# Performance work log

Hardware: AMD Instinct MI355X
Metric: run time of the kernel (lower is better)

## Reference

```python
import jax, jax.numpy as jnp
import numpy as np


def setup_inputs() -> dict:
    key = jax.random.key(0)
    k1, k2 = jax.random.split(key)
    queries = jax.random.normal(k1, (16, 1024, 256), dtype=jnp.float32)
    embedding = jax.random.normal(k2, (8192, 256), dtype=jnp.float32) * 0.02
    return {"queries": queries, "embedding": embedding}


def reference(queries, embedding):
    commitment_weight = 0.25
    # squared L2 distances: ||q||^2 + ||e||^2 - 2 q.e  -> [b, k, n]
    q_sq = jnp.sum(queries * queries, axis=-1, keepdims=True)          # [b,k,1]
    e_sq = jnp.sum(embedding * embedding, axis=-1)[None, None, :]      # [1,1,n]
    distances = q_sq + e_sq - 2.0 * jnp.einsum('bkc,nc->bkn', queries, embedding)
    code_indices = jnp.argmin(distances, axis=-1)                      # [b,k] int
    quantized = embedding[code_indices]                                # [b,k,c]
    commit_loss = jnp.mean((jax.lax.stop_gradient(queries) - quantized) ** 2)
    codebook_loss = jnp.mean((queries - jax.lax.stop_gradient(quantized)) ** 2)
    vq_loss = codebook_loss + commitment_weight * commit_loss
    # straight-through estimator
    quantized_st = queries + jax.lax.stop_gradient(quantized - queries)
    return (code_indices, quantized_st, vq_loss)
```

## Files before the change

### kernel.cpp

```cpp
#include <hip/hip_runtime.h>
#include <float.h>

typedef _Float16 half8 __attribute__((ext_vector_type(8)));
typedef _Float16 half4v __attribute__((ext_vector_type(4)));
typedef float f32x4 __attribute__((ext_vector_type(4)));

#define M_TOTAL 16384
#define N_CODES 8192
#define KDIM    256
#define BM 128
#define BN 256
#define BK 32
#define NK (KDIM / BK)
#define NB (N_CODES / BN)
#define TS 32
#define MARGIN 3.6e-3f
#define SQ_SCALE 512.0f
#define SE_SCALE 2048.0f
#define INV_PROD 1.9073486328125e-06f
#define RB 1024
#define LR_BLOCKS 32

#define PREP_Q_BLOCKS (M_TOTAL / 4)
#define PREP_E_BLOCKS (N_CODES / 4)
#define TR_BLOCKS ((N_CODES / 64) * (KDIM / 64))

__device__ __forceinline__ void prep_body(const float* __restrict__ src,
                                          _Float16* __restrict__ dst,
                                          float* __restrict__ sq, float scale,
                                          int row0, int tid) {
    {
        const int r = row0 + (tid >> 6);
        const int e4 = tid & 63;
        const float4 v = *(const float4*)(src + (size_t)r * KDIM + e4 * 4);
        const half4v h = {(_Float16)(v.x * scale), (_Float16)(v.y * scale),
                          (_Float16)(v.z * scale), (_Float16)(v.w * scale)};
        ((half4v*)(dst + (size_t)r * KDIM))[e4] = h;
    }
    if (tid < 64) {
        const int grp = tid >> 4;
        const int sub = tid & 15;
        const int row = row0 + grp;
        const float* p = src + (size_t)row * KDIM + (sub >> 3) * 128 + (sub & 7);
        float r;
        {
            #pragma clang fp contract(off)
            float v = p[0];
            r = v * v;
            #pragma unroll
            for (int k = 1; k < 16; k++) { const float w = p[k * 8]; r = r + w * w; }
        }
        const float t1 = r  + __shfl_xor(r,  1, 64);
        const float t2 = t1 + __shfl_xor(t1, 2, 64);
        const float t3 = t2 + __shfl_xor(t2, 4, 64);
        const float t4 = t3 + __shfl_xor(t3, 8, 64);
        if (sub == 0) sq[row] = t4;
    }
}

__global__ void prep_fused_kernel(const float* __restrict__ Q, const float* __restrict__ E,
                                  _Float16* __restrict__ Qh, _Float16* __restrict__ Eh,
                                  float* __restrict__ qsq, float* __restrict__ esq,
                                  float* __restrict__ ET,
                                  int* __restrict__ fcount, float* __restrict__ loss_slot) {
    __shared__ float tile[64][65];
    const int tid = threadIdx.x;
    const int b = blockIdx.x;
    if (b == 0 && tid == 0) { *fcount = 0; *loss_slot = 0.f; }
    if (b < PREP_Q_BLOCKS) {
        prep_body(Q, Qh, qsq, SQ_SCALE, b * 4, tid);
        return;
    }
    if (b < PREP_Q_BLOCKS + PREP_E_BLOCKS) {
        prep_body(E, Eh, esq, SE_SCALE, (b - PREP_Q_BLOCKS) * 4, tid);
        return;
    }
    const int idx = b - PREP_Q_BLOCKS - PREP_E_BLOCKS;
    const int n0 = (idx & 127) * 64;
    const int k0 = (idx >> 7) * 64;
    const int r = tid >> 4;
    const int c4 = tid & 15;
    #pragma unroll
    for (int p = 0; p < 4; p++) {
        const int row = p * 16 + r;
        const float4 v = *(const float4*)(E + (size_t)(n0 + row) * KDIM + k0 + c4 * 4);
        tile[row][c4 * 4 + 0] = v.x;
        tile[row][c4 * 4 + 1] = v.y;
        tile[row][c4 * 4 + 2] = v.z;
        tile[row][c4 * 4 + 3] = v.w;
    }
    __syncthreads();
    #pragma unroll
    for (int p = 0; p < 4; p++) {
        const int d = p * 16 + r;
        float4 o;
        o.x = tile[c4 * 4 + 0][d];
        o.y = tile[c4 * 4 + 1][d];
        o.z = tile[c4 * 4 + 2][d];
        o.w = tile[c4 * 4 + 3][d];
        *(float4*)(ET + (size_t)(k0 + d) * N_CODES + n0 + c4 * 4) = o;
    }
}

union SMemU {
    struct { _Float16 q[3][BM * TS]; _Float16 e[3][BN * TS]; } t;
    struct { unsigned k1[BM][2]; unsigned k2[BM][2]; } red;
};

__device__ __forceinline__ void gl_lds16(const void* g, void* lds) {
    __builtin_amdgcn_global_load_lds(
        (const __attribute__((address_space(1))) unsigned*)g,
        (__attribute__((address_space(3))) unsigned*)lds, 16, 0, 0);
}

__global__ __launch_bounds__(256, 2)
void mfma_top2_kernel(const _Float16* __restrict__ Qh, const _Float16* __restrict__ Eh,
                      const float* __restrict__ esq,
                      unsigned* __restrict__ k1s, unsigned* __restrict__ k2s) {
    __shared__ SMemU sm;
    const int tid = threadIdx.x;
    const int m0 = blockIdx.x * BM;
    const int n0 = blockIdx.y * BN;
    const int w = tid >> 6, lane = tid & 63;
    const int wm = w >> 1, wn = w & 1;
    const int qd = lane >> 4, c = lane & 15;

    const int lrow = lane >> 2;
    const int gsw = (lane & 3) ^ ((lane >> 3) & 3);
    const _Float16* qsrc = Qh + (size_t)(m0 + w * 32 + lrow) * KDIM + gsw * 8;
    const _Float16* esrc = Eh + (size_t)(n0 + w * 64 + lrow) * KDIM + gsw * 8;

    f32x4 acc[4][8];
    const f32x4 zero = {0.f, 0.f, 0.f, 0.f};
    #pragma unroll
    for (int mt = 0; mt < 4; mt++)
        #pragma unroll
        for (int nt = 0; nt < 8; nt++) acc[mt][nt] = zero;

    #define STAGE(buf, kofs) do {                                                  \
        _Float16* qdst = sm.t.q[buf] + w * 1024;                                   \
        _Float16* edst = sm.t.e[buf] + w * 2048;                                   \
        gl_lds16(qsrc + (kofs),             qdst);                                 \
        gl_lds16(qsrc + 16 * KDIM + (kofs), qdst + 512);                           \
        gl_lds16(esrc + (kofs),             edst);                                 \
        gl_lds16(esrc + 16 * KDIM + (kofs), edst + 512);                           \
        gl_lds16(esrc + 32 * KDIM + (kofs), edst + 1024);                          \
        gl_lds16(esrc + 48 * KDIM + (kofs), edst + 1536);                          \
    } while (0)

    STAGE(0, 0);
    STAGE(1, BK);
    STAGE(2, 2 * BK);
    asm volatile("s_waitcnt vmcnt(12)" ::: "memory");
    __builtin_amdgcn_s_barrier();

    const int csw = (c >> 1) & 3;

    #pragma unroll
    for (int ki = 0; ki < NK; ki++) {
        const int buf = ki % 3;
        const _Float16* bq = sm.t.q[buf];
        const _Float16* be = sm.t.e[buf];
        half8 qa[4];
        #pragma unroll
        for (int mt = 0; mt < 4; mt++)
            qa[mt] = *(const half8*)(bq + (wm * 64 + mt * 16 + c) * TS + (qd ^ csw) * 8);
        __builtin_amdgcn_s_setprio(1);
        #pragma unroll
        for (int nt = 0; nt < 8; nt++) {
            const half8 eh = *(const half8*)(be + (wn * 128 + nt * 16 + c) * TS + (qd ^ csw) * 8);
            #pragma unroll
            for (int mt = 0; mt < 4; mt++)
                acc[mt][nt] = __builtin_amdgcn_mfma_f32_16x16x32_f16(qa[mt], eh, acc[mt][nt], 0, 0, 0);
        }
        __builtin_amdgcn_s_setprio(0);
        if (ki == NK - 1) break;
        if (ki <= NK - 3) { asm volatile("s_waitcnt vmcnt(6)" ::: "memory"); }
        else              { asm volatile("s_waitcnt vmcnt(0)" ::: "memory"); }
        __builtin_amdgcn_s_barrier();
        if (ki + 3 < NK) STAGE(buf, (ki + 3) * BK);
    }
    #undef STAGE

    float es8[8];
    #pragma unroll
    for (int nt = 0; nt < 8; nt++) es8[nt] = esq[n0 + wn * 128 + nt * 16 + c] + 8.0f;

    unsigned k1[16], k2[16];
    #pragma unroll
    for (int i = 0; i < 16; i++) { k1[i] = 0xFFFFFFFFu; k2[i] = 0xFFFFFFFFu; }

    #pragma unroll
    for (int mt = 0; mt < 4; mt++)
        #pragma unroll
        for (int nt = 0; nt < 8; nt++) {
            const unsigned nl = (unsigned)(wn * 128 + nt * 16 + c);
            #pragma unroll
            for (int r = 0; r < 4; r++) {
                const int i = mt * 4 + r;
                const float d = fmaf(acc[mt][nt][r], -INV_PROD, es8[nt]);
                const unsigned k = (__float_as_uint(d) & 0xFFFFFF00u) | nl;
                const unsigned t = min(k1[i], k);
                k2[i] = min(k2[i], max(k1[i], k));
                k1[i] = t;
            }
        }
    #pragma unroll
    for (int s = 1; s < 16; s <<= 1) {
        #pragma unroll
        for (int i = 0; i < 16; i++) {
            const unsigned ok1 = (unsigned)__shfl_xor((int)k1[i], s, 64);
            const unsigned ok2 = (unsigned)__shfl_xor((int)k2[i], s, 64);
            const unsigned t = min(k1[i], ok1);
            k2[i] = min(min(k2[i], ok2), max(k1[i], ok1));
            k1[i] = t;
        }
    }
    __syncthreads();
    if (c == 0) {
        #pragma unroll
        for (int mt = 0; mt < 4; mt++)
            #pragma unroll
            for (int r = 0; r < 4; r++) {
                const int ml = wm * 64 + mt * 16 + qd * 4 + r;
                sm.red.k1[ml][wn] = k1[mt * 4 + r];
                sm.red.k2[ml][wn] = k2[mt * 4 + r];
            }
    }
    __syncthreads();
    if (tid < BM) {
        const unsigned a1 = sm.red.k1[tid][0], b1 = sm.red.k1[tid][1];
        const unsigned a2 = sm.red.k2[tid][0], b2 = sm.red.k2[tid][1];
        const size_t o = (size_t)(m0 + tid) * NB + blockIdx.y;
        k1s[o] = min(a1, b1);
        k2s[o] = min(min(a2, b2), max(a1, b1));
    }
}

__global__ void finalize_kernel(const float* __restrict__ Q, const float* __restrict__ E,
                                const unsigned* __restrict__ k1s, const unsigned* __restrict__ k2s,
                                int* __restrict__ fcount, int* __restrict__ flist,
                                float* __restrict__ ws_loss, float* __restrict__ out) {
    const int q = blockIdx.x * 4 + (threadIdx.x >> 6);
    const int lane = threadIdx.x & 63;
    unsigned d1 = 0xFFFFFF00u;
    unsigned d2 = 0xFFFFFF00u;
    int gi = 0x7FFFFFFF;
    if (lane < NB) {
        const unsigned k1 = k1s[(size_t)q * NB + lane];
        const unsigned k2 = k2s[(size_t)q * NB + lane];
        d1 = k1 & 0xFFFFFF00u;
        gi = lane * BN + (int)(k1 & 255u);
        d2 = k2 & 0xFFFFFF00u;
    }
    #pragma unroll
    for (int s = 1; s < 64; s <<= 1) {
        const unsigned od1 = (unsigned)__shfl_xor((int)d1, s, 64);
        const int      ogi = __shfl_xor(gi, s, 64);
        const unsigned od2 = (unsigned)__shfl_xor((int)d2, s, 64);
        const unsigned nd2 = min(min(d2, od2), max(d1, od1));
        const bool take = (od1 < d1) || (od1 == d1 && ogi < gi);
        d1 = take ? od1 : d1;
        gi = take ? ogi : gi;
        d2 = nd2;
    }
    if ((__uint_as_float(d2) - __uint_as_float(d1)) < MARGIN) {
        if (lane == 0) flist[atomicAdd(fcount, 1)] = q;
        return;
    }

    if (lane == 0) out[q] = (float)gi;
    const float4 qv = *(const float4*)(Q + (size_t)q * KDIM + lane * 4);
    const float4 ev = *(const float4*)(E + (size_t)gi * KDIM + lane * 4);
    float4 st;
    {
        #pragma clang fp contract(off)
        st.x = qv.x + (ev.x - qv.x);
        st.y = qv.y + (ev.y - qv.y);
        st.z = qv.z + (ev.z - qv.z);
        st.w = qv.w + (ev.w - qv.w);
    }
    *(float4*)(out + M_TOTAL + (size_t)q * KDIM + lane * 4) = st;

    const float dx = qv.x - ev.x, dy = qv.y - ev.y, dz = qv.z - ev.z, dw = qv.w - ev.w;
    float s = dx * dx + dy * dy + dz * dz + dw * dw;
    #pragma unroll
    for (int off = 32; off > 0; off >>= 1) s += __shfl_down(s, off);
    if (lane == 0) ws_loss[q] = s;
}

__global__ __launch_bounds__(256, 4)
void refine_kernel(const float* __restrict__ Q, const float* __restrict__ E,
                   const float* __restrict__ ET,
                   const float* __restrict__ qsq, const float* __restrict__ esq,
                   const int* __restrict__ fcount, const int* __restrict__ flist,
                   const unsigned* __restrict__ k1s,
                   float* __restrict__ ws_loss, float* __restrict__ out) {
    const int cnt = *fcount;
    const int tid = threadIdx.x;
    const int w = tid >> 6, lane = tid & 63;
    __shared__ float qs[KDIM];
    __shared__ unsigned cmask_sh;
    __shared__ float redv[4];
    __shared__ int   redi[4];

    for (int fi = blockIdx.x; fi < cnt; fi += RB) {
        const int q = flist[fi];
        __syncthreads();
        qs[tid] = Q[(size_t)q * KDIM + tid];
        if (w == 0) {
            unsigned k1 = 0xFFFFFF00u;
            if (lane < NB) k1 = k1s[(size_t)q * NB + lane];
            unsigned m = k1;
            #pragma unroll
            for (int s = 1; s < 64; s <<= 1)
                m = min(m, (unsigned)__shfl_xor((int)m, s, 64));
            const float thr = __uint_as_float(m & 0xFFFFFF00u) + MARGIN;
            const bool cand = (lane < NB) &&
                              (__uint_as_float(k1 & 0xFFFFFF00u) < thr);
            const unsigned long long bal = __ballot(cand);
            if (lane == 0) cmask_sh = (unsigned)bal;
        }
        __syncthreads();
        unsigned cmask = cmask_sh;
        const float qsv = qsq[q];
        float bv = FLT_MAX;
        int   bi = 0x7fffffff;
        while (cmask) {
            const int cb = __builtin_ctz(cmask);
            cmask &= cmask - 1;
            const int n = cb * BN + tid;
            float a = 0.f;
            #pragma unroll 8
            for (int k = 0; k < KDIM; k++)
                a = fmaf(qs[k], ET[(size_t)k * N_CODES + n], a);
            float d;
            {
                #pragma clang fp contract(off)
                const float t1 = qsv + esq[n];
                d = t1 - 2.0f * a;
            }
            if (d < bv || (d == bv && n < bi)) { bv = d; bi = n; }
        }
        #pragma unroll
        for (int s = 1; s < 64; s <<= 1) {
            const float ov = __shfl_xor(bv, s, 64);
            const int   oi = __shfl_xor(bi, s, 64);
            if (ov < bv || (ov == bv && oi < bi)) { bv = ov; bi = oi; }
        }
        if (lane == 0) { redv[w] = bv; redi[w] = bi; }
        __syncthreads();
        float fv = redv[0]; int fidx = redi[0];
        #pragma unroll
        for (int u = 1; u < 4; u++) {
            if (redv[u] < fv || (redv[u] == fv && redi[u] < fidx)) {
                fv = redv[u]; fidx = redi[u];
            }
        }
        if (w == 0) {
            if (lane == 0) out[q] = (float)fidx;
            const float4 qv = *(const float4*)(Q + (size_t)q * KDIM + lane * 4);
            const float4 ev = *(const float4*)(E + (size_t)fidx * KDIM + lane * 4);
            float4 st;
            {
                #pragma clang fp contract(off)
                st.x = qv.x + (ev.x - qv.x);
                st.y = qv.y + (ev.y - qv.y);
                st.z = qv.z + (ev.z - qv.z);
                st.w = qv.w + (ev.w - qv.w);
            }
            *(float4*)(out + M_TOTAL + (size_t)q * KDIM + lane * 4) = st;
            const float dx = qv.x - ev.x, dy = qv.y - ev.y;
            const float dz = qv.z - ev.z, dw = qv.w - ev.w;
            float s = dx * dx + dy * dy + dz * dz + dw * dw;
            #pragma unroll
            for (int off = 32; off > 0; off >>= 1) s += __shfl_down(s, off);
            if (lane == 0) ws_loss[q] = s;
        }
    }
}

__global__ void loss_reduce_kernel(const float* __restrict__ ws_loss, float* __restrict__ out) {
    const int tid = threadIdx.x;
    float s = 0.f;
    for (int i = blockIdx.x * 256 + tid; i < M_TOTAL; i += LR_BLOCKS * 256)
        s += ws_loss[i];
    #pragma unroll
    for (int off = 32; off > 0; off >>= 1) s += __shfl_down(s, off);
    __shared__ float ws[4];
    if ((tid & 63) == 0) ws[tid >> 6] = s;
    __syncthreads();
    if (tid == 0) {
        const float tot = (ws[0] + ws[1]) + (ws[2] + ws[3]);
        atomicAdd(out + M_TOTAL + (size_t)M_TOTAL * KDIM,
                  tot * (1.25f / (float)((size_t)M_TOTAL * KDIM)));
    }
}

extern "C" void kernel_launch(void* const* d_in, const int* in_sizes, int n_in,
                              void* d_out, int out_size, void* d_ws, size_t ws_size,
                              hipStream_t stream) {
    const float* Q = (const float*)d_in[0];
    const float* E = (const float*)d_in[1];
    float* out = (float*)d_out;

    char* ws = (char*)d_ws;
    _Float16* Qh  = (_Float16*)(ws);
    _Float16* Eh  = (_Float16*)(ws + (size_t)8  * 1024 * 1024);
    float* qsq    = (float*)   (ws + (size_t)12 * 1024 * 1024);
    float* esq    = qsq + M_TOTAL;
    unsigned* k1s = (unsigned*)(ws + (size_t)13 * 1024 * 1024);
    unsigned* k2s = (unsigned*)(ws + (size_t)17 * 1024 * 1024);
    int*   fcount = (int*)     (ws + (size_t)25 * 1024 * 1024);
    int*   flist  = fcount + 64;
    float* ws_loss= (float*)   (ws + (size_t)25 * 1024 * 1024 + 512 * 1024);
    float* ET     = (float*)   (ws + (size_t)26 * 1024 * 1024);
    float* loss_slot = out + M_TOTAL + (size_t)M_TOTAL * KDIM;

    prep_fused_kernel<<<PREP_Q_BLOCKS + PREP_E_BLOCKS + TR_BLOCKS, 256, 0, stream>>>(
        Q, E, Qh, Eh, qsq, esq, ET, fcount, loss_slot);

    mfma_top2_kernel<<<dim3(M_TOTAL / BM, N_CODES / BN), 256, 0, stream>>>(
        Qh, Eh, esq, k1s, k2s);

    finalize_kernel<<<M_TOTAL / 4, 256, 0, stream>>>(Q, E, k1s, k2s, fcount, flist, ws_loss, out);
    refine_kernel<<<RB, 256, 0, stream>>>(Q, E, ET, qsq, esq, fcount, flist, k1s, ws_loss, out);
    loss_reduce_kernel<<<LR_BLOCKS, 256, 0, stream>>>(ws_loss, out);
}
```

Measured before the change: 216.3 us.

## Fuse refine into finalize and switch GEMM to double-buffered LDS pipeline

Folds the separate refine kernel into the finalize kernel, so ambiguous queries are rescored in place by one wavefront using four columns per lane. This removes the atomic work list, one kernel launch and the flag round trip. The top-2 MFMA kernel moves from a triple-buffered, manually waitcnt-scheduled pipeline to a simpler double buffer with __syncthreads, drops setprio, and raises launch bounds to 3 blocks per CU. The lower LDS footprint may improve occupancy, but the shallower prefetch and full barriers can expose load latency. Per-wave refinement may also create load imbalance when candidates cluster.

New measurement: 342.9 us. 1.59x slower.

```diff
diff --git a/kernel.cpp b/kernel.cpp
--- a/kernel.cpp
+++ b/kernel.cpp
@@ -18,7 +18,6 @@
 #define SQ_SCALE 512.0f
 #define SE_SCALE 2048.0f
 #define INV_PROD 1.9073486328125e-06f
-#define RB 1024
 #define LR_BLOCKS 32
 
 #define PREP_Q_BLOCKS (M_TOTAL / 4)
@@ -61,12 +60,11 @@
 __global__ void prep_fused_kernel(const float* __restrict__ Q, const float* __restrict__ E,
                                   _Float16* __restrict__ Qh, _Float16* __restrict__ Eh,
                                   float* __restrict__ qsq, float* __restrict__ esq,
-                                  float* __restrict__ ET,
-                                  int* __restrict__ fcount, float* __restrict__ loss_slot) {
+                                  float* __restrict__ ET, float* __restrict__ loss_slot) {
     __shared__ float tile[64][65];
     const int tid = threadIdx.x;
     const int b = blockIdx.x;
-    if (b == 0 && tid == 0) { *fcount = 0; *loss_slot = 0.f; }
+    if (b == 0 && tid == 0) *loss_slot = 0.f;
     if (b < PREP_Q_BLOCKS) {
         prep_body(Q, Qh, qsq, SQ_SCALE, b * 4, tid);
         return;
@@ -103,7 +101,7 @@
 }
 
 union SMemU {
-    struct { _Float16 q[3][BM * TS]; _Float16 e[3][BN * TS]; } t;
+    struct { _Float16 q[2][BM * TS]; _Float16 e[2][BN * TS]; } t;
     struct { unsigned k1[BM][2]; unsigned k2[BM][2]; } red;
 };
 
@@ -113,7 +111,7 @@
         (__attribute__((address_space(3))) unsigned*)lds, 16, 0, 0);
 }
 
-__global__ __launch_bounds__(256, 2)
+__global__ __launch_bounds__(256, 3)
 void mfma_top2_kernel(const _Float16* __restrict__ Qh, const _Float16* __restrict__ Eh,
                       const float* __restrict__ esq,
                       unsigned* __restrict__ k1s, unsigned* __restrict__ k2s) {
@@ -149,23 +147,18 @@
     } while (0)
 
     STAGE(0, 0);
-    STAGE(1, BK);
-    STAGE(2, 2 * BK);
-    asm volatile("s_waitcnt vmcnt(12)" ::: "memory");
-    __builtin_amdgcn_s_barrier();
+    __syncthreads();
 
     const int csw = (c >> 1) & 3;
 
-    #pragma unroll
     for (int ki = 0; ki < NK; ki++) {
-        const int buf = ki % 3;
-        const _Float16* bq = sm.t.q[buf];
-        const _Float16* be = sm.t.e[buf];
+        if (ki + 1 < NK) STAGE((ki + 1) & 1, (ki + 1) * BK);
+        const _Float16* bq = sm.t.q[ki & 1];
+        const _Float16* be = sm.t.e[ki & 1];
         half8 qa[4];
         #pragma unroll
         for (int mt = 0; mt < 4; mt++)
             qa[mt] = *(const half8*)(bq + (wm * 64 + mt * 16 + c) * TS + (qd ^ csw) * 8);
-        __builtin_amdgcn_s_setprio(1);
         #pragma unroll
         for (int nt = 0; nt < 8; nt++) {
             const half8 eh = *(const half8*)(be + (wn * 128 + nt * 16 + c) * TS + (qd ^ csw) * 8);
@@ -173,12 +166,7 @@
             for (int mt = 0; mt < 4; mt++)
                 acc[mt][nt] = __builtin_amdgcn_mfma_f32_16x16x32_f16(qa[mt], eh, acc[mt][nt], 0, 0, 0);
         }
-        __builtin_amdgcn_s_setprio(0);
-        if (ki == NK - 1) break;
-        if (ki <= NK - 3) { asm volatile("s_waitcnt vmcnt(6)" ::: "memory"); }
-        else              { asm volatile("s_waitcnt vmcnt(0)" ::: "memory"); }
-        __builtin_amdgcn_s_barrier();
-        if (ki + 3 < NK) STAGE(buf, (ki + 3) * BK);
+        if (ki + 1 < NK) __syncthreads();
     }
     #undef STAGE
 
@@ -237,19 +225,26 @@
     }
 }
 
-__global__ void finalize_kernel(const float* __restrict__ Q, const float* __restrict__ E,
-                                const unsigned* __restrict__ k1s, const unsigned* __restrict__ k2s,
-                                int* __restrict__ fcount, int* __restrict__ flist,
-                                float* __restrict__ ws_loss, float* __restrict__ out) {
-    const int q = blockIdx.x * 4 + (threadIdx.x >> 6);
+__global__ __launch_bounds__(256, 4)
+void finalize_refine_kernel(const float* __restrict__ Q, const float* __restrict__ E,
+                            const float* __restrict__ ET,
+                            const float* __restrict__ qsq, const float* __restrict__ esq,
+                            const unsigned* __restrict__ k1s, const unsigned* __restrict__ k2s,
+                            float* __restrict__ ws_loss, float* __restrict__ out) {
+    __shared__ float qs[4][KDIM];
+    const int w = threadIdx.x >> 6;
     const int lane = threadIdx.x & 63;
+    const int q = blockIdx.x * 4 + w;
+
     unsigned d1 = 0xFFFFFF00u;
     unsigned d2 = 0xFFFFFF00u;
+    unsigned myk1 = 0xFFFFFF00u;
     int gi = 0x7FFFFFFF;
     if (lane < NB) {
         const unsigned k1 = k1s[(size_t)q * NB + lane];
         const unsigned k2 = k2s[(size_t)q * NB + lane];
-        d1 = k1 & 0xFFFFFF00u;
+        myk1 = k1 & 0xFFFFFF00u;
+        d1 = myk1;
         gi = lane * BN + (int)(k1 & 255u);
         d2 = k2 & 0xFFFFFF00u;
     }
@@ -264,13 +259,52 @@
         gi = take ? ogi : gi;
         d2 = nd2;
     }
+
+    const float4 qv = *(const float4*)(Q + (size_t)q * KDIM + lane * 4);
+
     if ((__uint_as_float(d2) - __uint_as_float(d1)) < MARGIN) {
-        if (lane == 0) flist[atomicAdd(fcount, 1)] = q;
-        return;
+        const float thr = __uint_as_float(d1) + MARGIN;
+        const bool cand = (lane < NB) && (__uint_as_float(myk1) < thr);
+        unsigned cmask = (unsigned)__ballot(cand);
+        *(float4*)&qs[w][lane * 4] = qv;
+        const float qsv = qsq[q];
+        float bv = FLT_MAX;
+        int   bi = 0x7fffffff;
+        while (cmask) {
+            const int cb = __builtin_ctz(cmask);
+            cmask &= cmask - 1;
+            const int nb4 = cb * BN + lane * 4;
+            float a0 = 0.f, a1 = 0.f, a2 = 0.f, a3 = 0.f;
+            for (int k = 0; k < KDIM; k++) {
+                const float qk = qs[w][k];
+                const float4 ev = *(const float4*)(ET + (size_t)k * N_CODES + nb4);
+                a0 = fmaf(qk, ev.x, a0);
+                a1 = fmaf(qk, ev.y, a1);
+                a2 = fmaf(qk, ev.z, a2);
+                a3 = fmaf(qk, ev.w, a3);
+            }
+            const float av[4] = {a0, a1, a2, a3};
+            #pragma unroll
+            for (int j = 0; j < 4; j++) {
+                float d;
+                {
+                    #pragma clang fp contract(off)
+                    const float t1 = qsv + esq[nb4 + j];
+                    d = t1 - 2.0f * av[j];
+                }
+                if (d < bv || (d == bv && nb4 + j < bi)) { bv = d; bi = nb4 + j; }
+            }
+        }
+        #pragma unroll
+        for (int s = 1; s < 64; s <<= 1) {
+            const float ov = __shfl_xor(bv, s, 64);
+            const int   oi = __shfl_xor(bi, s, 64);
+            if (ov < bv || (ov == bv && oi < bi)) { bv = ov; bi = oi; }
+        }
+        gi = bi;
     }
 
     if (lane == 0) out[q] = (float)gi;
-    const float4 qv = *(const float4*)(Q + (size_t)q * KDIM + lane * 4);
     const float4 ev = *(const float4*)(E + (size_t)gi * KDIM + lane * 4);
     float4 st;
     {
@@ -289,97 +323,6 @@
     if (lane == 0) ws_loss[q] = s;
 }
 
-__global__ __launch_bounds__(256, 4)
-void refine_kernel(const float* __restrict__ Q, const float* __restrict__ E,
-                   const float* __restrict__ ET,
-                   const float* __restrict__ qsq, const float* __restrict__ esq,
-                   const int* __restrict__ fcount, const int* __restrict__ flist,
-                   const unsigned* __restrict__ k1s,
-                   float* __restrict__ ws_loss, float* __restrict__ out) {
-    const int cnt = *fcount;
-    const int tid = threadIdx.x;
-    const int w = tid >> 6, lane = tid & 63;
-    __shared__ float qs[KDIM];
-    __shared__ unsigned cmask_sh;
-    __shared__ float redv[4];
-    __shared__ int   redi[4];
-
-    for (int fi = blockIdx.x; fi < cnt; fi += RB) {
-        const int q = flist[fi];
-        __syncthreads();
-        qs[tid] = Q[(size_t)q * KDIM + tid];
-        if (w == 0) {
-            unsigned k1 = 0xFFFFFF00u;
-            if (lane < NB) k1 = k1s[(size_t)q * NB + lane];
-            unsigned m = k1;
-            #pragma unroll
-            for (int s = 1; s < 64; s <<= 1)
-                m = min(m, (unsigned)__shfl_xor((int)m, s, 64));
-            const float thr = __uint_as_float(m & 0xFFFFFF00u) + MARGIN;
-            const bool cand = (lane < NB) &&
-                              (__uint_as_float(k1 & 0xFFFFFF00u) < thr);
-            const unsigned long long bal = __ballot(cand);
-            if (lane == 0) cmask_sh = (unsigned)bal;
-        }
-        __syncthreads();
-        unsigned cmask = cmask_sh;
-        const float qsv = qsq[q];
-        float bv = FLT_MAX;
-        int   bi = 0x7fffffff;
-        while (cmask) {
-            const int cb = __builtin_ctz(cmask);
-            cmask &= cmask - 1;
-            const int n = cb * BN + tid;
-            float a = 0.f;
-            #pragma unroll 8
-            for (int k = 0; k < KDIM; k++)
-                a = fmaf(qs[k], ET[(size_t)k * N_CODES + n], a);
-            float d;
-            {
-                #pragma clang fp contract(off)
-                const float t1 = qsv + esq[n];
-                d = t1 - 2.0f * a;
-            }
-            if (d < bv || (d == bv && n < bi)) { bv = d; bi = n; }
-        }
-        #pragma unroll
-        for (int s = 1; s < 64; s <<= 1) {
-            const float ov = __shfl_xor(bv, s, 64);
-            const int   oi = __shfl_xor(bi, s, 64);
-            if (ov < bv || (ov == bv && oi < bi)) { bv = ov; bi = oi; }
-        }
-        if (lane == 0) { redv[w] = bv; redi[w] = bi; }
-        __syncthreads();
-        float fv = redv[0]; int fidx = redi[0];
-        #pragma unroll
-        for (int u = 1; u < 4; u++) {
-            if (redv[u] < fv || (redv[u] == fv && redi[u] < fidx)) {
-                fv = redv[u]; fidx = redi[u];
-            }
-        }
-        if (w == 0) {
-            if (lane == 0) out[q] = (float)fidx;
-            const float4 qv = *(const float4*)(Q + (size_t)q * KDIM + lane * 4);
-            const float4 ev = *(const float4*)(E + (size_t)fidx * KDIM + lane * 4);
-            float4 st;
-            {
-                #pragma clang fp contract(off)
-                st.x = qv.x + (ev.x - qv.x);
-                st.y = qv.y + (ev.y - qv.y);
-                st.z = qv.z + (ev.z - qv.z);
-                st.w = qv.w + (ev.w - qv.w);
-            }
-            *(float4*)(out + M_TOTAL + (size_t)q * KDIM + lane * 4) = st;
-            const float dx = qv.x - ev.x, dy = qv.y - ev.y;
-            const float dz = qv.z - ev.z, dw = qv.w - ev.w;
-            float s = dx * dx + dy * dy + dz * dz + dw * dw;
-            #pragma unroll
-            for (int off = 32; off > 0; off >>= 1) s += __shfl_down(s, off);
-            if (lane == 0) ws_loss[q] = s;
-        }
-    }
-}
-
 __global__ void loss_reduce_kernel(const float* __restrict__ ws_loss, float* __restrict__ out) {
     const int tid = threadIdx.x;
     float s = 0.f;
@@ -411,19 +354,18 @@
     float* esq    = qsq + M_TOTAL;
     unsigned* k1s = (unsigned*)(ws + (size_t)13 * 1024 * 1024);
     unsigned* k2s = (unsigned*)(ws + (size_t)17 * 1024 * 1024);
-    int*   fcount = (int*)     (ws + (size_t)25 * 1024 * 1024);
-    int*   flist  = fcount + 64;
     float* ws_loss= (float*)   (ws + (size_t)25 * 1024 * 1024 + 512 * 1024);
     float* ET     = (float*)   (ws + (size_t)26 * 1024 * 1024);
     float* loss_slot = out + M_TOTAL + (size_t)M_TOTAL * KDIM;
 
     prep_fused_kernel<<<PREP_Q_BLOCKS + PREP_E_BLOCKS + TR_BLOCKS, 256, 0, stream>>>(
-        Q, E, Qh, Eh, qsq, esq, ET, fcount, loss_slot);
+        Q, E, Qh, Eh, qsq, esq, ET, loss_slot);
 
     mfma_top2_kernel<<<dim3(M_TOTAL / BM, N_CODES / BN), 256, 0, stream>>>(
         Qh, Eh, esq, k1s, k2s);
 
-    finalize_kernel<<<M_TOTAL / 4, 256, 0, stream>>>(Q, E, k1s, k2s, fcount, flist, ws_loss, out);
-    refine_kernel<<<RB, 256, 0, stream>>>(Q, E, ET, qsq, esq, fcount, flist, k1s, ws_loss, out);
+    finalize_refine_kernel<<<M_TOTAL / 4, 256, 0, stream>>>(
+        Q, E, ET, qsq, esq, k1s, k2s, ws_loss, out);
+
     loss_reduce_kernel<<<LR_BLOCKS, 256, 0, stream>>>(ws_loss, out);
 }
```
